# Optimization experiments

Hardware: AMD Instinct MI355X
Metric: run time of the kernel (lower is better)

The kernel has to match this reference:

```python
import jax, jax.numpy as jnp
import numpy as np

N, IN_FEAT, EMBED, HEADS = 4096, 256, 256, 8
HEAD_DIM = EMBED // HEADS
SCALING = HEAD_DIM ** -0.5


def setup_inputs() -> dict:
    key = jax.random.key(0)
    ks = jax.random.split(key, 8)
    s = 1.0 / np.sqrt(IN_FEAT)
    return {
        'x': jax.random.normal(ks[0], (N, IN_FEAT), jnp.float32),
        'adj': jax.random.randint(ks[1], (N, N), 0, 2, jnp.int32),
        'Wq': jax.random.normal(ks[2], (EMBED, IN_FEAT), jnp.float32) * s,
        'bq': jnp.zeros((EMBED,), jnp.float32),
        'Wk': jax.random.normal(ks[3], (EMBED, IN_FEAT), jnp.float32) * s,
        'bk': jnp.zeros((EMBED,), jnp.float32),
        'Wv': jax.random.normal(ks[4], (EMBED, IN_FEAT), jnp.float32) * s,
        'bv': jnp.zeros((EMBED,), jnp.float32),
    }


def reference(x, adj, Wq, bq, Wk, bk, Wv, bv):
    n = x.shape[0]
    # project and split heads: [H, N, Dh]
    Q = (x @ Wq.T + bq).reshape(n, HEADS, HEAD_DIM).transpose(1, 0, 2)
    K = (x @ Wk.T + bk).reshape(n, HEADS, HEAD_DIM).transpose(1, 0, 2)
    V = (x @ Wv.T + bv).reshape(n, HEADS, HEAD_DIM).transpose(1, 0, 2)
    # leaky_relu score (torch default slope 0.01), then scale
    scores = jax.nn.leaky_relu(jnp.einsum('hqd,hkd->hqk', Q, K), 0.01) * SCALING
    # additive adjacency mask broadcast over heads
    scores = scores + jnp.where(adj > 0, 0.0, -jnp.inf)
    attn = jax.nn.softmax(scores, axis=-1)
    # dropout is identity in eval mode
    mixed = jnp.einsum('hqk,hkd->hqd', attn, jax.nn.softmax(V, axis=-1))
    return V - mixed
```

## Files before the change

### kernel.cpp

```cpp
#include <hip/hip_runtime.h>
#include <hip/hip_bf16.h>
#include <math.h>

#define N_NODES 4096
#define NIN     256
#define EMBED   256
#define HEADS   8
#define HEAD_DIM 32
#define QKSCALE 0.2550610017f

typedef float f32x16 __attribute__((ext_vector_type(16)));
typedef short bf16x8 __attribute__((ext_vector_type(8)));
typedef unsigned int u32x2 __attribute__((ext_vector_type(2)));
typedef unsigned short ushort_t;

static __device__ __forceinline__ ushort_t f2bf(float x) {
  unsigned u = __float_as_uint(x);
  unsigned r = (u + 0x7fffu + ((u >> 16) & 1u)) >> 16;
  return (ushort_t)r;
}
static __device__ __forceinline__ float bf2f(ushort_t b) {
  return __uint_as_float((unsigned)b << 16);
}
static __device__ __forceinline__ unsigned cvt_pk_bf16(float lo, float hi) {
  unsigned r;
  asm("v_cvt_pk_bf16_f32 %0, %1, %2" : "=v"(r) : "v"(lo), "v"(hi));
  return r;
}
static __device__ __forceinline__ float fast_exp2(float x) {
  float r;
  asm("v_exp_f32 %0, %1" : "=v"(r) : "v"(x));
  return r;
}

static __device__ __forceinline__ void half_swap(unsigned a, unsigned b, bool hi,
                                                 unsigned& r0, unsigned& r1) {
#if __has_builtin(__builtin_amdgcn_permlane32_swap)
  u32x2 s = __builtin_amdgcn_permlane32_swap(a, b, false, false);
  r0 = s[0]; r1 = s[1];
#else
  unsigned ax = (unsigned)__shfl_xor((int)a, 32);
  unsigned bx = (unsigned)__shfl_xor((int)b, 32);
  r0 = hi ? bx : a;
  r1 = hi ? b  : ax;
#endif
}

__global__ __launch_bounds__(256) void pack_adj(const int* __restrict__ adj,
                                                unsigned int* __restrict__ bitsT) {
  int q = blockIdx.x;
  int wave = threadIdx.x >> 6, lane = threadIdx.x & 63;
  #pragma unroll
  for (int i = 0; i < 16; ++i) {
    int g64 = wave * 16 + i;
    int k = g64 * 64 + lane;
    int v = adj[(size_t)q * N_NODES + k];
    unsigned long long b = __ballot(v > 0);
    if (lane == 0) {
      bitsT[(size_t)(2 * g64)     * N_NODES + q] = (unsigned int)b;
      bitsT[(size_t)(2 * g64 + 1) * N_NODES + q] = (unsigned int)(b >> 32);
    }
  }
}

__global__ __launch_bounds__(256) void split_x(const float* __restrict__ x,
    ushort_t* __restrict__ xh, ushort_t* __restrict__ xl) {
  int idx = blockIdx.x * 256 + threadIdx.x;
  float4 v = ((const float4*)x)[idx];
  union { ushort_t u[4]; unsigned long long q; } hb, lb;
  float c[4] = {v.x, v.y, v.z, v.w};
  #pragma unroll
  for (int j = 0; j < 4; ++j) {
    hb.u[j] = f2bf(c[j]);
    lb.u[j] = f2bf(c[j] - bf2f(hb.u[j]));
  }
  *(unsigned long long*)(xh + (size_t)idx * 4) = hb.q;
  *(unsigned long long*)(xl + (size_t)idx * 4) = lb.q;
}

__global__ __launch_bounds__(256) void split_w(const float* __restrict__ Wq,
    const float* __restrict__ Wk, const float* __restrict__ Wv,
    ushort_t* __restrict__ Wh, ushort_t* __restrict__ Wl) {
  int idx = blockIdx.x * 256 + threadIdx.x;
  int row = idx >> 6;
  const float* src = row < 256 ? Wq : (row < 512 ? Wk : Wv);
  float4 v = ((const float4*)(src + (size_t)(row & 255) * NIN))[idx & 63];
  union { ushort_t u[4]; unsigned long long q; } hb, lb;
  float c[4] = {v.x, v.y, v.z, v.w};
  #pragma unroll
  for (int j = 0; j < 4; ++j) {
    hb.u[j] = f2bf(c[j]);
    lb.u[j] = f2bf(c[j] - bf2f(hb.u[j]));
  }
  *(unsigned long long*)(Wh + (size_t)idx * 4) = hb.q;
  *(unsigned long long*)(Wl + (size_t)idx * 4) = lb.q;
}

__global__ __launch_bounds__(256) void qkv_mfma(
    const ushort_t* __restrict__ xh, const ushort_t* __restrict__ xl,
    const ushort_t* __restrict__ Wh, const ushort_t* __restrict__ Wl,
    const float* __restrict__ bq, const float* __restrict__ bk,
    const float* __restrict__ bv,
    ushort_t* __restrict__ Qph, ushort_t* __restrict__ Qpl,
    ushort_t* __restrict__ Kph, ushort_t* __restrict__ Kpl,
    float* __restrict__ Vo) {
  __shared__ float ts[4][32][33];
  int lane = threadIdx.x & 63, w = threadIdx.x >> 6;
  int c = lane & 31, g = lane >> 5;
  int mt = blockIdx.x;
  int et = blockIdx.y * 4 + w;

  const ushort_t* wha = Wh + (size_t)(et * 32 + c) * NIN + g * 8;
  const ushort_t* wla = Wl + (size_t)(et * 32 + c) * NIN + g * 8;
  const ushort_t* xha = xh + (size_t)(mt * 32 + c) * NIN + g * 8;
  const ushort_t* xla = xl + (size_t)(mt * 32 + c) * NIN + g * 8;

  f32x16 acc;
  #pragma unroll
  for (int i = 0; i < 16; ++i) acc[i] = 0.f;
  #pragma unroll 4
  for (int s = 0; s < 16; ++s) {
    bf16x8 ah = *(const bf16x8*)(wha + s * 16);
    bf16x8 al = *(const bf16x8*)(wla + s * 16);
    bf16x8 bh = *(const bf16x8*)(xha + s * 16);
    bf16x8 bl = *(const bf16x8*)(xla + s * 16);
    acc = __builtin_amdgcn_mfma_f32_32x32x16_bf16(ah, bh, acc, 0, 0, 0);
    acc = __builtin_amdgcn_mfma_f32_32x32x16_bf16(ah, bl, acc, 0, 0, 0);
    acc = __builtin_amdgcn_mfma_f32_32x32x16_bf16(al, bh, acc, 0, 0, 0);
  }

  int mat = et >> 3, h = et & 7;
  const float* bias = mat == 0 ? bq : (mat == 1 ? bk : bv);
  float scl = mat == 0 ? QKSCALE : 1.0f;
  #pragma unroll
  for (int r = 0; r < 16; ++r) {
    int erow = (r & 3) + 8 * (r >> 2) + 4 * g;
    ts[w][erow][c] = (acc[r] + bias[h * 32 + erow]) * scl;
  }
  if (mat < 2) {
    ushort_t* Ph = mat == 0 ? Qph : Kph;
    ushort_t* Pl = mat == 0 ? Qpl : Kpl;
    #pragma unroll
    for (int sl = 0; sl < 2; ++sl) {
      union { ushort_t u[8]; bf16x8 v; } hbv, lbv;
      #pragma unroll
      for (int j = 0; j < 8; ++j) {
        float v = ts[w][sl * 16 + g * 8 + j][c];
        hbv.u[j] = f2bf(v);
        lbv.u[j] = f2bf(v - bf2f(hbv.u[j]));
      }
      size_t dst = (((size_t)(h * 128 + mt) * 2 + sl) * 64 + lane) * 8;
      *(bf16x8*)(Ph + dst) = hbv.v;
      *(bf16x8*)(Pl + dst) = lbv.v;
    }
  } else {
    #pragma unroll
    for (int i = 0; i < 16; ++i) {
      int flat = lane + i * 64;
      int ml = flat >> 5, el = flat & 31;
      Vo[(size_t)(mt * 32 + ml) * EMBED + h * 32 + el] = ts[w][el][ml];
    }
  }
}

__global__ __launch_bounds__(256) void sv_softmax_t(const float* __restrict__ V,
    ushort_t* __restrict__ SVph, ushort_t* __restrict__ SVpl) {
  __shared__ float sv[32][257];
  int tile = blockIdx.x;
  int n0 = tile * 32;
  int t = threadIdx.x;
  for (int i = 0; i < 32; ++i) sv[i][t] = V[(size_t)(n0 + i) * EMBED + t];
  __syncthreads();
  int node = t & 31, hh = t >> 5;
  float mx = -INFINITY;
  #pragma unroll
  for (int d = 0; d < 32; ++d) mx = fmaxf(mx, sv[node][hh * 32 + d]);
  float s = 0.f;
  #pragma unroll
  for (int d = 0; d < 32; ++d) s += __expf(sv[node][hh * 32 + d] - mx);
  float inv = 1.f / s;
  #pragma unroll
  for (int d = 0; d < 32; ++d)
    sv[node][hh * 32 + d] = __expf(sv[node][hh * 32 + d] - mx) * inv;
  __syncthreads();
  #pragma unroll
  for (int i = 0; i < 4; ++i) {
    int fid = t + i * 256;
    int h = fid >> 7, sl = (fid >> 6) & 1, ln = fid & 63;
    int g = ln >> 5, c = ln & 31;
    union { ushort_t u[8]; bf16x8 v; } hb, lb;
    #pragma unroll
    for (int j = 0; j < 8; ++j) {
      int n = sl * 16 + g * 8 + j;
      float v = sv[n][h * 32 + c];
      hb.u[j] = f2bf(v);
      lb.u[j] = f2bf(v - bf2f(hb.u[j]));
    }
    size_t dst = (((size_t)(h * 128 + tile) * 2 + sl) * 64 + ln) * 8;
    *(bf16x8*)(SVph + dst) = hb.v;
    *(bf16x8*)(SVpl + dst) = lb.v;
  }
}

__global__ __launch_bounds__(512) void attn32(
    const ushort_t* __restrict__ Qph, const ushort_t* __restrict__ Qpl,
    const ushort_t* __restrict__ Kph, const ushort_t* __restrict__ Kpl,
    const ushort_t* __restrict__ SVph, const ushort_t* __restrict__ SVpl,
    const unsigned int* __restrict__ bitsT, const float* __restrict__ V,
    float* __restrict__ out) {
  __shared__ float o_s[8][32][32];
  __shared__ float l_s[8][32];

  int lane = threadIdx.x & 63;
  int wid  = threadIdx.x >> 6;
  int col  = lane & 31;
  int g    = lane >> 5;
  bool hi  = (g != 0);
  int h  = blockIdx.y;
  int qt = blockIdx.x;
  int q0 = qt * 32;
  int q  = q0 + col;

  size_t qbase = ((size_t)(h * 128 + qt) * 2) * 512 + lane * 8;
  bf16x8 qbh0 = *(const bf16x8*)(Qph + qbase);
  bf16x8 qbh1 = *(const bf16x8*)(Qph + qbase + 512);
  bf16x8 qbl0 = *(const bf16x8*)(Qpl + qbase);
  bf16x8 qbl1 = *(const bf16x8*)(Qpl + qbase + 512);

  f32x16 o;
  #pragma unroll
  for (int i = 0; i < 16; ++i) o[i] = 0.f;
  float lsum = 0.f;

  #pragma unroll 2
  for (int t = 0; t < 16; ++t) {
    int tile = wid * 16 + t;
    size_t kb = ((size_t)(h * 128 + tile) * 2) * 512 + lane * 8;
    bf16x8 kah0 = *(const bf16x8*)(Kph + kb);
    bf16x8 kah1 = *(const bf16x8*)(Kph + kb + 512);
    bf16x8 kal0 = *(const bf16x8*)(Kpl + kb);
    bf16x8 kal1 = *(const bf16x8*)(Kpl + kb + 512);
    unsigned int mw = bitsT[(size_t)tile * N_NODES + q] >> (4 * g);

    f32x16 st;
    #pragma unroll
    for (int i = 0; i < 16; ++i) st[i] = 0.f;
    __builtin_amdgcn_s_setprio(1);
    st = __builtin_amdgcn_mfma_f32_32x32x16_bf16(kah0, qbh0, st, 0, 0, 0);
    st = __builtin_amdgcn_mfma_f32_32x32x16_bf16(kah1, qbh1, st, 0, 0, 0);
    st = __builtin_amdgcn_mfma_f32_32x32x16_bf16(kah0, qbl0, st, 0, 0, 0);
    st = __builtin_amdgcn_mfma_f32_32x32x16_bf16(kah1, qbl1, st, 0, 0, 0);
    st = __builtin_amdgcn_mfma_f32_32x32x16_bf16(kal0, qbh0, st, 0, 0, 0);
    st = __builtin_amdgcn_mfma_f32_32x32x16_bf16(kal1, qbh1, st, 0, 0, 0);
    __builtin_amdgcn_s_setprio(0);

    float p[16];
    #pragma unroll
    for (int r = 0; r < 16; ++r) {
      float v = st[r];
      float pe = fast_exp2(fmaxf(v, 0.01f * v));
      bool on = (mw >> ((r & 3) + 8 * (r >> 2))) & 1;
      float pv = on ? pe : 0.f;
      p[r] = pv;
      lsum += pv;
    }

    unsigned int w[8];
    #pragma unroll
    for (int i = 0; i < 8; ++i) w[i] = cvt_pk_bf16(p[2 * i], p[2 * i + 1]);
    unsigned s02a, s02b, s13a, s13b, s46a, s46b, s57a, s57b;
    half_swap(w[0], w[2], hi, s02a, s02b);
    half_swap(w[1], w[3], hi, s13a, s13b);
    half_swap(w[4], w[6], hi, s46a, s46b);
    half_swap(w[5], w[7], hi, s57a, s57b);
    union { unsigned int u[4]; bf16x8 v; } pa0, pa1;
    pa0.u[0] = s02a; pa0.u[1] = s13a; pa0.u[2] = s02b; pa0.u[3] = s13b;
    pa1.u[0] = s46a; pa1.u[1] = s57a; pa1.u[2] = s46b; pa1.u[3] = s57b;

    size_t sb = ((size_t)(h * 128 + tile) * 2) * 512 + lane * 8;
    bf16x8 svh0 = *(const bf16x8*)(SVph + sb);
    bf16x8 svh1 = *(const bf16x8*)(SVph + sb + 512);
    bf16x8 svl0 = *(const bf16x8*)(SVpl + sb);
    bf16x8 svl1 = *(const bf16x8*)(SVpl + sb + 512);
    __builtin_amdgcn_s_setprio(1);
    o = __builtin_amdgcn_mfma_f32_32x32x16_bf16(pa0.v, svh0, o, 0, 0, 0);
    o = __builtin_amdgcn_mfma_f32_32x32x16_bf16(pa1.v, svh1, o, 0, 0, 0);
    o = __builtin_amdgcn_mfma_f32_32x32x16_bf16(pa0.v, svl0, o, 0, 0, 0);
    o = __builtin_amdgcn_mfma_f32_32x32x16_bf16(pa1.v, svl1, o, 0, 0, 0);
    __builtin_amdgcn_s_setprio(0);
  }

  float Lt = lsum + __shfl_xor(lsum, 32);
  #pragma unroll
  for (int r = 0; r < 16; ++r) {
    int ql = (r & 3) + 8 * (r >> 2) + 4 * g;
    o_s[wid][ql][col] = o[r];
  }
  if (lane < 32) l_s[wid][col] = Lt;
  __syncthreads();

  #pragma unroll
  for (int i = 0; i < 2; ++i) {
    int idx = threadIdx.x + i * 512;
    int ql = idx >> 5, d = idx & 31;
    float O = 0.f, L = 0.f;
    #pragma unroll
    for (int w2 = 0; w2 < 8; ++w2) {
      O += o_s[w2][ql][d];
      L += l_s[w2][ql];
    }
    int qq = q0 + ql;
    out[((size_t)h * N_NODES + qq) * HEAD_DIM + d] =
        V[(size_t)qq * EMBED + h * HEAD_DIM + d] - O / L;
  }
}

extern "C" void kernel_launch(void* const* d_in, const int* in_sizes, int n_in,
                              void* d_out, int out_size, void* d_ws, size_t ws_size,
                              hipStream_t stream) {
  const float* x   = (const float*)d_in[0];
  const int*   adj = (const int*)d_in[1];
  const float* Wq  = (const float*)d_in[2];
  const float* bq  = (const float*)d_in[3];
  const float* Wk  = (const float*)d_in[4];
  const float* bk  = (const float*)d_in[5];
  const float* Wv  = (const float*)d_in[6];
  const float* bv  = (const float*)d_in[7];
  float* out = (float*)d_out;

  char* ws = (char*)d_ws;
  ushort_t*     Qph  = (ushort_t*)(ws);
  ushort_t*     Qpl  = (ushort_t*)(ws + ((size_t)2  << 20));
  ushort_t*     Kph  = (ushort_t*)(ws + ((size_t)4  << 20));
  ushort_t*     Kpl  = (ushort_t*)(ws + ((size_t)6  << 20));
  ushort_t*     SVph = (ushort_t*)(ws + ((size_t)8  << 20));
  ushort_t*     SVpl = (ushort_t*)(ws + ((size_t)10 << 20));
  float*        V    = (float*)(ws + ((size_t)12 << 20));
  unsigned int* bits = (unsigned int*)(ws + ((size_t)16 << 20));
  ushort_t*     xh   = (ushort_t*)(ws + ((size_t)18 << 20));
  ushort_t*     xl   = (ushort_t*)(ws + ((size_t)20 << 20));
  ushort_t*     Wh   = (ushort_t*)(ws + ((size_t)22 << 20));
  ushort_t*     Wl   = (ushort_t*)(ws + ((size_t)22 << 20) + 393216);

  pack_adj<<<dim3(N_NODES), 256, 0, stream>>>(adj, bits);
  split_x<<<dim3((N_NODES * NIN / 4) / 256), 256, 0, stream>>>(x, xh, xl);
  split_w<<<dim3((768 * NIN / 4) / 256), 256, 0, stream>>>(Wq, Wk, Wv, Wh, Wl);
  qkv_mfma<<<dim3(N_NODES / 32, 6), 256, 0, stream>>>(
      xh, xl, Wh, Wl, bq, bk, bv, Qph, Qpl, Kph, Kpl, V);
  sv_softmax_t<<<dim3(N_NODES / 32), 256, 0, stream>>>(V, SVph, SVpl);
  attn32<<<dim3(N_NODES / 32, HEADS), 512, 0, stream>>>(
      Qph, Qpl, Kph, Kpl, SVph, SVpl, bits, V, out);
}
```

Baseline: 219.3 us.

## Share K/V tiles across four query tiles via double-buffered LDS staging

The attention kernel is restructured so each 512-thread block handles four query tiles for one head. The eight waves split into four query groups and two key halves instead of eight key slices of one query tile. K and softmax(V) tiles are cooperatively loaded once per block into a double-buffered LDS stage and reused by the four query waves, cutting global/L2 traffic for K/V fourfold. The cost is a __syncthreads per key tile and a smaller grid of 256 blocks, which may leave some CUs underused, and the cross-wave reduction shrinks to two partials.

```diff
diff --git a/kernel.cpp b/kernel.cpp
--- a/kernel.cpp
+++ b/kernel.cpp
@@ -208,7 +208,8 @@
     const ushort_t* __restrict__ SVph, const ushort_t* __restrict__ SVpl,
     const unsigned int* __restrict__ bitsT, const float* __restrict__ V,
     float* __restrict__ out) {
-  __shared__ float o_s[8][32][32];
+  __shared__ ushort_t stage[2][2][4][1024];
+  __shared__ float o_s[4][32][32];
   __shared__ float l_s[8][32];
 
   int lane = threadIdx.x & 63;
@@ -216,30 +217,60 @@
   int col  = lane & 31;
   int g    = lane >> 5;
   bool hi  = (g != 0);
-  int h  = blockIdx.y;
-  int qt = blockIdx.x;
-  int q0 = qt * 32;
-  int q  = q0 + col;
-
-  size_t qbase = ((size_t)(h * 128 + qt) * 2) * 512 + lane * 8;
-  bf16x8 qbh0 = *(const bf16x8*)(Qph + qbase);
-  bf16x8 qbh1 = *(const bf16x8*)(Qph + qbase + 512);
-  bf16x8 qbl0 = *(const bf16x8*)(Qpl + qbase);
-  bf16x8 qbl1 = *(const bf16x8*)(Qpl + qbase + 512);
+  int wq   = wid & 3;
+  int wkc  = wid >> 2;
+  int bid  = blockIdx.x;
+  int h    = bid & 7;
+  int qblk = bid >> 3;
+  int qt_w = qblk * 4 + wq;
+  int q    = qt_w * 32 + col;
+
+  int sw = wid >> 2, sc = wid & 3;
+  const ushort_t* mysrc =
+      (sc == 0 ? Kph : sc == 1 ? Kpl : sc == 2 ? SVph : SVpl) +
+      (size_t)(h * 128) * 1024;
+
+  size_t qb = (size_t)(h * 128 + qt_w) * 1024 + lane * 8;
+  bf16x8 qbh0 = *(const bf16x8*)(Qph + qb);
+  bf16x8 qbh1 = *(const bf16x8*)(Qph + qb + 512);
+  bf16x8 qbl0 = *(const bf16x8*)(Qpl + qb);
+  bf16x8 qbl1 = *(const bf16x8*)(Qpl + qb + 512);
 
   f32x16 o;
   #pragma unroll
   for (int i = 0; i < 16; ++i) o[i] = 0.f;
   float lsum = 0.f;
 
-  #pragma unroll 2
-  for (int t = 0; t < 16; ++t) {
-    int tile = wid * 16 + t;
-    size_t kb = ((size_t)(h * 128 + tile) * 2) * 512 + lane * 8;
-    bf16x8 kah0 = *(const bf16x8*)(Kph + kb);
-    bf16x8 kah1 = *(const bf16x8*)(Kph + kb + 512);
-    bf16x8 kal0 = *(const bf16x8*)(Kpl + kb);
-    bf16x8 kal1 = *(const bf16x8*)(Kpl + kb + 512);
+  {
+    const ushort_t* s = mysrc + (size_t)(sw * 64) * 1024;
+    bf16x8 p0 = *(const bf16x8*)(s + lane * 8);
+    bf16x8 p1 = *(const bf16x8*)(s + 512 + lane * 8);
+    ushort_t* d = &stage[0][sw][sc][0];
+    *(bf16x8*)(d + lane * 8) = p0;
+    *(bf16x8*)(d + 512 + lane * 8) = p1;
+  }
+  int cur = 0;
+
+  for (int t = 0; t < 64; ++t) {
+    __syncthreads();
+
+    bf16x8 r0, r1;
+    if (t < 63) {
+      const ushort_t* s = mysrc + (size_t)(sw * 64 + t + 1) * 1024;
+      r0 = *(const bf16x8*)(s + lane * 8);
+      r1 = *(const bf16x8*)(s + 512 + lane * 8);
+    }
+
+    int tile = wkc * 64 + t;
+    const ushort_t* kh  = &stage[cur][wkc][0][0];
+    const ushort_t* kl  = &stage[cur][wkc][1][0];
+    const ushort_t* shv = &stage[cur][wkc][2][0];
+    const ushort_t* slv = &stage[cur][wkc][3][0];
+
+    bf16x8 kah0 = *(const bf16x8*)(kh + lane * 8);
+    bf16x8 kah1 = *(const bf16x8*)(kh + 512 + lane * 8);
+    bf16x8 kal0 = *(const bf16x8*)(kl + lane * 8);
+    bf16x8 kal1 = *(const bf16x8*)(kl + 512 + lane * 8);
     unsigned int mw = bitsT[(size_t)tile * N_NODES + q] >> (4 * g);
 
     f32x16 st;
@@ -277,41 +308,45 @@
     pa0.u[0] = s02a; pa0.u[1] = s13a; pa0.u[2] = s02b; pa0.u[3] = s13b;
     pa1.u[0] = s46a; pa1.u[1] = s57a; pa1.u[2] = s46b; pa1.u[3] = s57b;
 
-    size_t sb = ((size_t)(h * 128 + tile) * 2) * 512 + lane * 8;
-    bf16x8 svh0 = *(const bf16x8*)(SVph + sb);
-    bf16x8 svh1 = *(const bf16x8*)(SVph + sb + 512);
-    bf16x8 svl0 = *(const bf16x8*)(SVpl + sb);
-    bf16x8 svl1 = *(const bf16x8*)(SVpl + sb + 512);
+    bf16x8 svh0 = *(const bf16x8*)(shv + lane * 8);
+    bf16x8 svh1 = *(const bf16x8*)(shv + 512 + lane * 8);
+    bf16x8 svl0 = *(const bf16x8*)(slv + lane * 8);
+    bf16x8 svl1 = *(const bf16x8*)(slv + 512 + lane * 8);
     __builtin_amdgcn_s_setprio(1);
     o = __builtin_amdgcn_mfma_f32_32x32x16_bf16(pa0.v, svh0, o, 0, 0, 0);
     o = __builtin_amdgcn_mfma_f32_32x32x16_bf16(pa1.v, svh1, o, 0, 0, 0);
     o = __builtin_amdgcn_mfma_f32_32x32x16_bf16(pa0.v, svl0, o, 0, 0, 0);
     o = __builtin_amdgcn_mfma_f32_32x32x16_bf16(pa1.v, svl1, o, 0, 0, 0);
     __builtin_amdgcn_s_setprio(0);
+
+    if (t < 63) {
+      ushort_t* d = &stage[cur ^ 1][sw][sc][0];
+      *(bf16x8*)(d + lane * 8) = r0;
+      *(bf16x8*)(d + 512 + lane * 8) = r1;
+      cur ^= 1;
+    }
   }
 
   float Lt = lsum + __shfl_xor(lsum, 32);
-  #pragma unroll
-  for (int r = 0; r < 16; ++r) {
-    int ql = (r & 3) + 8 * (r >> 2) + 4 * g;
-    o_s[wid][ql][col] = o[r];
-  }
   if (lane < 32) l_s[wid][col] = Lt;
+  if (wkc == 1) {
+    #pragma unroll
+    for (int r = 0; r < 16; ++r) {
+      int qr = (r & 3) + 8 * (r >> 2) + 4 * g;
+      o_s[wq][qr][col] = o[r];
+    }
+  }
   __syncthreads();
-
-  #pragma unroll
-  for (int i = 0; i < 2; ++i) {
-    int idx = threadIdx.x + i * 512;
-    int ql = idx >> 5, d = idx & 31;
-    float O = 0.f, L = 0.f;
-    #pragma unroll
-    for (int w2 = 0; w2 < 8; ++w2) {
-      O += o_s[w2][ql][d];
-      L += l_s[w2][ql];
-    }
-    int qq = q0 + ql;
-    out[((size_t)h * N_NODES + qq) * HEAD_DIM + d] =
-        V[(size_t)qq * EMBED + h * HEAD_DIM + d] - O / L;
+  if (wkc == 0) {
+    #pragma unroll
+    for (int r = 0; r < 16; ++r) {
+      int qr = (r & 3) + 8 * (r >> 2) + 4 * g;
+      float O = o[r] + o_s[wq][qr][col];
+      float L = l_s[wq][qr] + l_s[4 + wq][qr];
+      int qg = qblk * 128 + wq * 32 + qr;
+      float vv = V[(size_t)qg * EMBED + h * 32 + col];
+      out[((size_t)h * N_NODES + qg) * HEAD_DIM + col] = vv - O / L;
+    }
   }
 }
 
@@ -348,6 +383,6 @@
   qkv_mfma<<<dim3(N_NODES / 32, 6), 256, 0, stream>>>(
       xh, xl, Wh, Wl, bq, bk, bv, Qph, Qpl, Kph, Kpl, V);
   sv_softmax_t<<<dim3(N_NODES / 32), 256, 0, stream>>>(V, SVph, SVpl);
-  attn32<<<dim3(N_NODES / 32, HEADS), 512, 0, stream>>>(
+  attn32<<<dim3(256), 512, 0, stream>>>(
       Qph, Qpl, Kph, Kpl, SVph, SVpl, bits, V, out);
 }
```

Result: slower. 232.8 us (+6.2%).
